# Kernel optimization log

Hardware: AMD Instinct MI355X
Metric: run time of the kernel (lower is better)

Reference implementation:

```python
import jax, jax.numpy as jnp
import numpy as np

EPS = 1e-5

def _bn_relu(y, s, b, m, v):
    # eval-mode BatchNorm1d over channel dim (axis=1) followed by ReLU
    inv = s / jnp.sqrt(v + EPS)
    return jax.nn.relu((y - m[None, :, None]) * inv[None, :, None] + b[None, :, None])

def setup_inputs() -> dict:
    key = jax.random.key(0)
    ks = jax.random.split(key, 24)
    B, C, N, CL = 4, 256, 4096, 32  # CL = C // latent
    x = jax.random.normal(ks[0], (B, C, N), dtype=jnp.float32)
    def w(k, o, i):
        return jax.random.normal(k, (o, i), dtype=jnp.float32) * (1.0 / np.sqrt(i))
    def bn(k0, k1, d):
        s = 1.0 + 0.1 * jax.random.normal(k0, (d,), dtype=jnp.float32)
        b = 0.1 * jax.random.normal(k1, (d,), dtype=jnp.float32)
        m = 0.1 * jax.random.normal(jax.random.fold_in(k0, 7), (d,), dtype=jnp.float32)
        v = 0.5 + jax.random.uniform(jax.random.fold_in(k1, 7), (d,), dtype=jnp.float32)
        return s, b, m, v
    w1 = w(ks[1], CL, C); w2 = w(ks[2], CL, C); w3 = w(ks[3], CL, C)
    w_out = w(ks[4], C, CL)
    bn1_s, bn1_b, bn1_m, bn1_v = bn(ks[5], ks[6], CL)
    bn2_s, bn2_b, bn2_m, bn2_v = bn(ks[7], ks[8], CL)
    bn3_s, bn3_b, bn3_m, bn3_v = bn(ks[9], ks[10], CL)
    bn4_s, bn4_b, bn4_m, bn4_v = bn(ks[11], ks[12], C)
    gamma = jnp.float32(0.5)  # torch inits to 0 (identity output); use 0.5 for a nontrivial baseline
    return dict(x=x, w1=w1, w2=w2, w3=w3, w_out=w_out,
                bn1_s=bn1_s, bn1_b=bn1_b, bn1_m=bn1_m, bn1_v=bn1_v,
                bn2_s=bn2_s, bn2_b=bn2_b, bn2_m=bn2_m, bn2_v=bn2_v,
                bn3_s=bn3_s, bn3_b=bn3_b, bn3_m=bn3_m, bn3_v=bn3_v,
                bn4_s=bn4_s, bn4_b=bn4_b, bn4_m=bn4_m, bn4_v=bn4_v,
                gamma=gamma)

def reference(x, w1, w2, w3, w_out,
              bn1_s, bn1_b, bn1_m, bn1_v,
              bn2_s, bn2_b, bn2_m, bn2_v,
              bn3_s, bn3_b, bn3_m, bn3_v,
              bn4_s, bn4_b, bn4_m, bn4_v,
              gamma):
    # conv1x1 == channel matmul: [o,c] x [b,c,n] -> [b,o,n]
    out1 = _bn_relu(jnp.einsum('oc,bcn->bon', w1, x), bn1_s, bn1_b, bn1_m, bn1_v)  # [b,CL,n]
    out2 = _bn_relu(jnp.einsum('oc,bcn->bon', w2, x), bn2_s, bn2_b, bn2_m, bn2_v)  # [b,CL,n]
    out3 = _bn_relu(jnp.einsum('oc,bcn->bon', w3, x), bn3_s, bn3_b, bn3_m, bn3_v)  # [b,CL,n]
    # attention[b,i,j] = softmax_j( out1[b,:,i] . out2[b,:,j] )
    scores = jnp.einsum('bci,bcj->bij', out1, out2)          # [b,n,n]
    attn = jax.nn.softmax(scores, axis=-1)
    # attention output: bmm(out3, attn^T) -> [b,CL,n]
    agg = jnp.einsum('bck,bmk->bcm', out3, attn)
    out = _bn_relu(jnp.einsum('oc,bcn->bon', w_out, agg), bn4_s, bn4_b, bn4_m, bn4_v)  # [b,C,n]
    return gamma * out + x
```

## Files before the change

### kernel.cpp

```cpp
#include <hip/hip_runtime.h>
#include <hip/hip_bf16.h>
#include <math.h>

#define BATCH 4
#define CDIM 256
#define NDIM 4096
#define CLD 32
#define EPSBN 1e-5f
#define SPLITS 8
#define KEYS_PER_WAVE (NDIM / SPLITS)
#define LOG2E 1.4426950408889634f
#define NT (NDIM / 32)

typedef unsigned short u16;
typedef unsigned int u32;
typedef __attribute__((ext_vector_type(8))) short bf16x8;
typedef __attribute__((ext_vector_type(16))) float f32x16;
typedef __attribute__((ext_vector_type(4))) u32 u32x4;
typedef __attribute__((ext_vector_type(2))) u32 u32x2;

__device__ inline u16 f2bf(float x) {
    return __builtin_bit_cast(u16, __float2bfloat16(x));
}
__device__ inline u32 pack_bf16x2(float a, float b) {
    return (u32)f2bf(a) | ((u32)f2bf(b) << 16);
}
__device__ inline bf16x8 pack8(float4 a, float4 b) {
    u32x4 u;
    u.x = pack_bf16x2(a.x, a.y); u.y = pack_bf16x2(a.z, a.w);
    u.z = pack_bf16x2(b.x, b.y); u.w = pack_bf16x2(b.z, b.w);
    return __builtin_bit_cast(bf16x8, u);
}

__global__ __launch_bounds__(256) void proj_qkv(
    const float* __restrict__ x,
    const float* __restrict__ w1, const float* __restrict__ w2, const float* __restrict__ w3,
    const float* __restrict__ b1s, const float* __restrict__ b1b, const float* __restrict__ b1m, const float* __restrict__ b1v,
    const float* __restrict__ b2s, const float* __restrict__ b2b, const float* __restrict__ b2m, const float* __restrict__ b2v,
    const float* __restrict__ b3s, const float* __restrict__ b3b, const float* __restrict__ b3m, const float* __restrict__ b3v,
    u16* __restrict__ qo, u16* __restrict__ ko, u16* __restrict__ vo)
{
    __shared__ float2 sbn[32];

    const int tid  = threadIdx.x;
    const int lane = tid & 63;
    const int col  = lane & 31;
    const int hi   = lane >> 5;
    const int wv   = tid >> 6;
    const int mat  = blockIdx.y;
    const int b    = blockIdx.z;
    const int tl   = blockIdx.x * 4 + wv;
    const int n0   = tl * 32;

    if (tid < 32) {
        const float* ps = (mat == 0) ? b1s : (mat == 1) ? b2s : b3s;
        const float* pb = (mat == 0) ? b1b : (mat == 1) ? b2b : b3b;
        const float* pm = (mat == 0) ? b1m : (mat == 1) ? b2m : b3m;
        const float* pv = (mat == 0) ? b1v : (mat == 1) ? b2v : b3v;
        float inv  = ps[tid] / sqrtf(pv[tid] + EPSBN);
        float bias = pb[tid] - pm[tid] * inv;
        if (mat == 0) { inv *= LOG2E; bias *= LOG2E; }
        sbn[tid] = make_float2(inv, bias);
    }
    __syncthreads();

    const float* wb = ((mat == 0) ? w1 : (mat == 1) ? w2 : w3) + (size_t)col * CDIM + 8 * hi;
    bf16x8 wf[16];
#pragma unroll
    for (int f = 0; f < 16; ++f) {
        float4 a = *reinterpret_cast<const float4*>(wb + 16 * f);
        float4 c = *reinterpret_cast<const float4*>(wb + 16 * f + 4);
        wf[f] = pack8(a, c);
    }

    const float* xb = x + (size_t)b * CDIM * NDIM + n0 + col;

    f32x16 acc = {0.f,0.f,0.f,0.f, 0.f,0.f,0.f,0.f, 0.f,0.f,0.f,0.f, 0.f,0.f,0.f,0.f};
#pragma unroll
    for (int f = 0; f < 16; ++f) {
        float xv[8];
#pragma unroll
        for (int i = 0; i < 8; ++i)
            xv[i] = xb[(size_t)(16 * f + 8 * hi + i) * NDIM];
        u32x4 u;
        u.x = pack_bf16x2(xv[0], xv[1]); u.y = pack_bf16x2(xv[2], xv[3]);
        u.z = pack_bf16x2(xv[4], xv[5]); u.w = pack_bf16x2(xv[6], xv[7]);
        acc = __builtin_amdgcn_mfma_f32_32x32x16_bf16(wf[f], __builtin_bit_cast(bf16x8, u), acc, 0, 0, 0);
    }

    if (mat < 2) {
        u16* dst = ((mat == 0) ? qo : ko) + ((size_t)b * NDIM + n0 + col) * CLD;
#pragma unroll
        for (int g2 = 0; g2 < 4; ++g2) {
            float y[4];
#pragma unroll
            for (int j = 0; j < 4; ++j) {
                int o = 8 * g2 + 4 * hi + j;
                float2 ib = sbn[o];
                y[j] = fmaxf(fmaf(acc[4 * g2 + j], ib.x, ib.y), 0.f);
            }
            u32x2 s;
            s.x = pack_bf16x2(y[0], y[1]); s.y = pack_bf16x2(y[2], y[3]);
            *reinterpret_cast<u32x2*>(dst + 8 * g2 + 4 * hi) = s;
        }
    } else {
        int p = col;
        int q2 = (p >> 2) & 3;
        if (q2 == 1 || q2 == 2) p ^= 12;
        u16* base = vo + (size_t)(b * NT + tl) * 1024 + p;
#pragma unroll
        for (int r = 0; r < 16; ++r) {
            int d = (r & 3) + 8 * (r >> 2) + 4 * hi;
            float2 ib = sbn[d];
            base[d * 32] = f2bf(fmaxf(fmaf(acc[r], ib.x, ib.y), 0.f));
        }
    }
}

__global__ __launch_bounds__(512, 4) void attn_mfma(
    const u16* __restrict__ q, const u16* __restrict__ k, const u16* __restrict__ v,
    float* __restrict__ agg)
{
    __shared__ float o_lds[SPLITS][32][32];
    __shared__ float l_lds[SPLITS][32];

    const int tid  = threadIdx.x;
    const int lane = tid & 63;
    const int w    = tid >> 6;
    const int b    = blockIdx.y;
    const int q0   = blockIdx.x * 32;
    const int col  = lane & 31;
    const int hi   = lane >> 5;

    const u16* qp = q + ((size_t)b * NDIM + q0 + col) * CLD + 8 * hi;
    bf16x8 qf0 = *reinterpret_cast<const bf16x8*>(qp);
    bf16x8 qf1 = *reinterpret_cast<const bf16x8*>(qp + 16);

    f32x16 o = {0.f,0.f,0.f,0.f, 0.f,0.f,0.f,0.f, 0.f,0.f,0.f,0.f, 0.f,0.f,0.f,0.f};
    float l_lane = 0.f;

    const int kstart = w * KEYS_PER_WAVE;
    const u16* kb = k + (size_t)b * NDIM * CLD;
    const u16* vb = v + (size_t)(b * NT) * 1024 + (size_t)col * 32 + 8 * hi;

    for (int kt = 0; kt < KEYS_PER_WAVE; kt += 64) {
        const int k0 = kstart + kt;
        const u16* kp1 = kb + (size_t)(k0 + col) * CLD + 8 * hi;
        bf16x8 kf10 = *reinterpret_cast<const bf16x8*>(kp1);
        bf16x8 kf11 = *reinterpret_cast<const bf16x8*>(kp1 + 16);
        const u16* kp2 = kp1 + 32 * CLD;
        bf16x8 kf20 = *reinterpret_cast<const bf16x8*>(kp2);
        bf16x8 kf21 = *reinterpret_cast<const bf16x8*>(kp2 + 16);

        const u16* vp = vb + (size_t)(k0 >> 5) * 1024;
        bf16x8 vf10 = *reinterpret_cast<const bf16x8*>(vp);
        bf16x8 vf11 = *reinterpret_cast<const bf16x8*>(vp + 16);
        bf16x8 vf20 = *reinterpret_cast<const bf16x8*>(vp + 1024);
        bf16x8 vf21 = *reinterpret_cast<const bf16x8*>(vp + 1040);

        f32x16 sa = {0.f,0.f,0.f,0.f, 0.f,0.f,0.f,0.f, 0.f,0.f,0.f,0.f, 0.f,0.f,0.f,0.f};
        f32x16 sb = {0.f,0.f,0.f,0.f, 0.f,0.f,0.f,0.f, 0.f,0.f,0.f,0.f, 0.f,0.f,0.f,0.f};
        sa = __builtin_amdgcn_mfma_f32_32x32x16_bf16(kf10, qf0, sa, 0, 0, 0);
        sa = __builtin_amdgcn_mfma_f32_32x32x16_bf16(kf11, qf1, sa, 0, 0, 0);
        sb = __builtin_amdgcn_mfma_f32_32x32x16_bf16(kf20, qf0, sb, 0, 0, 0);
        sb = __builtin_amdgcn_mfma_f32_32x32x16_bf16(kf21, qf1, sb, 0, 0, 0);

        float psum = 0.f;
#pragma unroll
        for (int r = 0; r < 16; ++r) { sa[r] = exp2f(sa[r]); psum += sa[r]; }
#pragma unroll
        for (int r = 0; r < 16; ++r) { sb[r] = exp2f(sb[r]); psum += sb[r]; }
        l_lane += psum;

        u32x4 p10, p11, p20, p21;
        p10.x = pack_bf16x2(sa[0],  sa[1]);  p10.y = pack_bf16x2(sa[2],  sa[3]);
        p10.z = pack_bf16x2(sa[4],  sa[5]);  p10.w = pack_bf16x2(sa[6],  sa[7]);
        p11.x = pack_bf16x2(sa[8],  sa[9]);  p11.y = pack_bf16x2(sa[10], sa[11]);
        p11.z = pack_bf16x2(sa[12], sa[13]); p11.w = pack_bf16x2(sa[14], sa[15]);
        p20.x = pack_bf16x2(sb[0],  sb[1]);  p20.y = pack_bf16x2(sb[2],  sb[3]);
        p20.z = pack_bf16x2(sb[4],  sb[5]);  p20.w = pack_bf16x2(sb[6],  sb[7]);
        p21.x = pack_bf16x2(sb[8],  sb[9]);  p21.y = pack_bf16x2(sb[10], sb[11]);
        p21.z = pack_bf16x2(sb[12], sb[13]); p21.w = pack_bf16x2(sb[14], sb[15]);

        o = __builtin_amdgcn_mfma_f32_32x32x16_bf16(vf10, __builtin_bit_cast(bf16x8, p10), o, 0, 0, 0);
        o = __builtin_amdgcn_mfma_f32_32x32x16_bf16(vf11, __builtin_bit_cast(bf16x8, p11), o, 0, 0, 0);
        o = __builtin_amdgcn_mfma_f32_32x32x16_bf16(vf20, __builtin_bit_cast(bf16x8, p20), o, 0, 0, 0);
        o = __builtin_amdgcn_mfma_f32_32x32x16_bf16(vf21, __builtin_bit_cast(bf16x8, p21), o, 0, 0, 0);
    }

#pragma unroll
    for (int r = 0; r < 16; ++r) {
        int d = (r & 3) + 8 * (r >> 2) + 4 * hi;
        o_lds[w][d][col] = o[r];
    }
    float l_tot = l_lane + __shfl_xor(l_lane, 32);
    if (hi == 0) l_lds[w][col] = l_tot;
    __syncthreads();

    {
        const int qq = tid & 31;
        const int d0 = tid >> 5;
        float den = 0.f;
#pragma unroll
        for (int s = 0; s < SPLITS; ++s) den += l_lds[s][qq];
        float inv = 1.f / den;
#pragma unroll
        for (int dd = 0; dd < 2; ++dd) {
            int d = d0 + 16 * dd;
            float a2 = 0.f;
#pragma unroll
            for (int s = 0; s < SPLITS; ++s) a2 += o_lds[s][d][qq];
            agg[((size_t)b * CLD + d) * NDIM + q0 + qq] = a2 * inv;
        }
    }
}

__global__ __launch_bounds__(256) void out_proj(
    const float* __restrict__ agg, const float* __restrict__ wo,
    const float* __restrict__ b4s, const float* __restrict__ b4b,
    const float* __restrict__ b4m, const float* __restrict__ b4v,
    const float* __restrict__ x, const float* __restrict__ gamma,
    float* __restrict__ out)
{
    const int tid   = threadIdx.x;
    const int lane  = tid & 63;
    const int b     = blockIdx.y;
    const int w     = __builtin_amdgcn_readfirstlane(tid >> 6);
    const int obase = blockIdx.z * 32 + w * 8;
    const int n     = blockIdx.x * 256 + lane * 4;

    float4 acc[8];
#pragma unroll
    for (int o = 0; o < 8; ++o) acc[o] = make_float4(0.f, 0.f, 0.f, 0.f);

    const float* wbase = wo + (size_t)obase * CLD;

#pragma unroll 2
    for (int c = 0; c < CLD; c += 4) {
        float4 wq[8];
#pragma unroll
        for (int o = 0; o < 8; ++o)
            wq[o] = *reinterpret_cast<const float4*>(wbase + o * CLD + c);
        float4 av[4];
#pragma unroll
        for (int cc = 0; cc < 4; ++cc)
            av[cc] = *reinterpret_cast<const float4*>(agg + ((size_t)b * CLD + c + cc) * NDIM + n);
#pragma unroll
        for (int cc = 0; cc < 4; ++cc) {
#pragma unroll
            for (int o = 0; o < 8; ++o) {
                float wv = (cc == 0) ? wq[o].x : (cc == 1) ? wq[o].y : (cc == 2) ? wq[o].z : wq[o].w;
                acc[o].x = fmaf(wv, av[cc].x, acc[o].x);
                acc[o].y = fmaf(wv, av[cc].y, acc[o].y);
                acc[o].z = fmaf(wv, av[cc].z, acc[o].z);
                acc[o].w = fmaf(wv, av[cc].w, acc[o].w);
            }
        }
    }

    const float gm = gamma[0];
#pragma unroll
    for (int o = 0; o < 8; ++o) {
        int oo = obase + o;
        float inv = b4s[oo] / sqrtf(b4v[oo] + EPSBN);
        float bi  = b4b[oo] - b4m[oo] * inv;
        const size_t idx = ((size_t)b * CDIM + oo) * NDIM + n;
        float4 xv = *reinterpret_cast<const float4*>(x + idx);
        float4 r;
        r.x = fmaf(gm, fmaxf(fmaf(acc[o].x, inv, bi), 0.f), xv.x);
        r.y = fmaf(gm, fmaxf(fmaf(acc[o].y, inv, bi), 0.f), xv.y);
        r.z = fmaf(gm, fmaxf(fmaf(acc[o].z, inv, bi), 0.f), xv.z);
        r.w = fmaf(gm, fmaxf(fmaf(acc[o].w, inv, bi), 0.f), xv.w);
        *reinterpret_cast<float4*>(out + idx) = r;
    }
}

extern "C" void kernel_launch(void* const* d_in, const int* in_sizes, int n_in,
                              void* d_out, int out_size, void* d_ws, size_t ws_size,
                              hipStream_t stream) {
    const float* x   = (const float*)d_in[0];
    const float* w1  = (const float*)d_in[1];
    const float* w2  = (const float*)d_in[2];
    const float* w3  = (const float*)d_in[3];
    const float* wo  = (const float*)d_in[4];
    const float* b1s = (const float*)d_in[5];
    const float* b1b = (const float*)d_in[6];
    const float* b1m = (const float*)d_in[7];
    const float* b1v = (const float*)d_in[8];
    const float* b2s = (const float*)d_in[9];
    const float* b2b = (const float*)d_in[10];
    const float* b2m = (const float*)d_in[11];
    const float* b2v = (const float*)d_in[12];
    const float* b3s = (const float*)d_in[13];
    const float* b3b = (const float*)d_in[14];
    const float* b3m = (const float*)d_in[15];
    const float* b3v = (const float*)d_in[16];
    const float* b4s = (const float*)d_in[17];
    const float* b4b = (const float*)d_in[18];
    const float* b4m = (const float*)d_in[19];
    const float* b4v = (const float*)d_in[20];
    const float* gm  = (const float*)d_in[21];
    float* out = (float*)d_out;

    char* W = (char*)d_ws;
    u16* qbf = (u16*)W;
    u16* kbf = (u16*)(W + (1u << 20));
    u16* vbf = (u16*)(W + (2u << 20));
    float* agg = (float*)(W + (3u << 20));

    dim3 gp(32, 3, BATCH);
    proj_qkv<<<gp, 256, 0, stream>>>(x, w1, w2, w3,
                                     b1s, b1b, b1m, b1v,
                                     b2s, b2b, b2m, b2v,
                                     b3s, b3b, b3m, b3v,
                                     qbf, kbf, vbf);

    dim3 ga(NDIM / 32, BATCH);
    attn_mfma<<<ga, 512, 0, stream>>>(qbf, kbf, vbf, agg);

    dim3 go(NDIM / 256, BATCH, 8);
    out_proj<<<go, 256, 0, stream>>>(agg, wo, b4s, b4b, b4m, b4v, x, gm, out);
}
```

Before: 51.02 us.

## Fuse output projection, BN and residual into the attention kernel epilogue

Merges the separate out_proj kernel into the attention kernel. After the split-K reduction, normalized attention outputs are packed to bf16 in LDS, and each wave runs two MFMAs to project 32 latent channels to 32 of the 256 output channels. BN4, ReLU and gamma are applied and staged through LDS, then added to x with coalesced float4 stores. This removes the fp32 agg round trip through global memory and one kernel launch, but the output projection now runs in bf16 instead of fp32 and adds LDS use and extra barriers to the attention kernel.

```diff
diff --git a/kernel.cpp b/kernel.cpp
--- a/kernel.cpp
+++ b/kernel.cpp
@@ -117,12 +117,18 @@
     }
 }
 
-__global__ __launch_bounds__(512, 4) void attn_mfma(
+__global__ __launch_bounds__(512, 4) void attn_fused(
     const u16* __restrict__ q, const u16* __restrict__ k, const u16* __restrict__ v,
-    float* __restrict__ agg)
+    const float* __restrict__ wo,
+    const float* __restrict__ b4s, const float* __restrict__ b4b,
+    const float* __restrict__ b4m, const float* __restrict__ b4v,
+    const float* __restrict__ x, const float* __restrict__ gamma,
+    float* __restrict__ out)
 {
     __shared__ float o_lds[SPLITS][32][32];
     __shared__ float l_lds[SPLITS][32];
+    __shared__ u16  p_lds[32][40];
+    __shared__ float2 sbn4[CDIM];
 
     const int tid  = threadIdx.x;
     const int lane = tid & 63;
@@ -131,6 +137,11 @@
     const int q0   = blockIdx.x * 32;
     const int col  = lane & 31;
     const int hi   = lane >> 5;
+
+    if (tid < CDIM) {
+        float inv = b4s[tid] / sqrtf(b4v[tid] + EPSBN);
+        sbn4[tid] = make_float2(inv, b4b[tid] - b4m[tid] * inv);
+    }
 
     const u16* qp = q + ((size_t)b * NDIM + q0 + col) * CLD + 8 * hi;
     bf16x8 qf0 = *reinterpret_cast<const bf16x8*>(qp);
@@ -199,79 +210,56 @@
 
     {
         const int qq = tid & 31;
-        const int d0 = tid >> 5;
+        const int dp = tid >> 5;
         float den = 0.f;
 #pragma unroll
         for (int s = 0; s < SPLITS; ++s) den += l_lds[s][qq];
         float inv = 1.f / den;
-#pragma unroll
-        for (int dd = 0; dd < 2; ++dd) {
-            int d = d0 + 16 * dd;
-            float a2 = 0.f;
-#pragma unroll
-            for (int s = 0; s < SPLITS; ++s) a2 += o_lds[s][d][qq];
-            agg[((size_t)b * CLD + d) * NDIM + q0 + qq] = a2 * inv;
+        float a0 = 0.f, a1 = 0.f;
+#pragma unroll
+        for (int s = 0; s < SPLITS; ++s) {
+            a0 += o_lds[s][2 * dp][qq];
+            a1 += o_lds[s][2 * dp + 1][qq];
         }
-    }
-}
-
-__global__ __launch_bounds__(256) void out_proj(
-    const float* __restrict__ agg, const float* __restrict__ wo,
-    const float* __restrict__ b4s, const float* __restrict__ b4b,
-    const float* __restrict__ b4m, const float* __restrict__ b4v,
-    const float* __restrict__ x, const float* __restrict__ gamma,
-    float* __restrict__ out)
-{
-    const int tid   = threadIdx.x;
-    const int lane  = tid & 63;
-    const int b     = blockIdx.y;
-    const int w     = __builtin_amdgcn_readfirstlane(tid >> 6);
-    const int obase = blockIdx.z * 32 + w * 8;
-    const int n     = blockIdx.x * 256 + lane * 4;
-
-    float4 acc[8];
-#pragma unroll
-    for (int o = 0; o < 8; ++o) acc[o] = make_float4(0.f, 0.f, 0.f, 0.f);
-
-    const float* wbase = wo + (size_t)obase * CLD;
-
-#pragma unroll 2
-    for (int c = 0; c < CLD; c += 4) {
-        float4 wq[8];
-#pragma unroll
-        for (int o = 0; o < 8; ++o)
-            wq[o] = *reinterpret_cast<const float4*>(wbase + o * CLD + c);
-        float4 av[4];
-#pragma unroll
-        for (int cc = 0; cc < 4; ++cc)
-            av[cc] = *reinterpret_cast<const float4*>(agg + ((size_t)b * CLD + c + cc) * NDIM + n);
-#pragma unroll
-        for (int cc = 0; cc < 4; ++cc) {
-#pragma unroll
-            for (int o = 0; o < 8; ++o) {
-                float wv = (cc == 0) ? wq[o].x : (cc == 1) ? wq[o].y : (cc == 2) ? wq[o].z : wq[o].w;
-                acc[o].x = fmaf(wv, av[cc].x, acc[o].x);
-                acc[o].y = fmaf(wv, av[cc].y, acc[o].y);
-                acc[o].z = fmaf(wv, av[cc].z, acc[o].z);
-                acc[o].w = fmaf(wv, av[cc].w, acc[o].w);
-            }
+        *reinterpret_cast<u32*>(&p_lds[qq][2 * dp]) = pack_bf16x2(a0 * inv, a1 * inv);
+    }
+    __syncthreads();
+
+    const int o0 = w * 32;
+    const float* wp = wo + (size_t)(o0 + col) * CLD + 8 * hi;
+    bf16x8 wf0 = pack8(*reinterpret_cast<const float4*>(wp),
+                       *reinterpret_cast<const float4*>(wp + 4));
+    bf16x8 wf1 = pack8(*reinterpret_cast<const float4*>(wp + 16),
+                       *reinterpret_cast<const float4*>(wp + 20));
+    bf16x8 pf0 = *reinterpret_cast<const bf16x8*>(&p_lds[col][8 * hi]);
+    bf16x8 pf1 = *reinterpret_cast<const bf16x8*>(&p_lds[col][16 + 8 * hi]);
+
+    f32x16 acc = {0.f,0.f,0.f,0.f, 0.f,0.f,0.f,0.f, 0.f,0.f,0.f,0.f, 0.f,0.f,0.f,0.f};
+    acc = __builtin_amdgcn_mfma_f32_32x32x16_bf16(wf0, pf0, acc, 0, 0, 0);
+    acc = __builtin_amdgcn_mfma_f32_32x32x16_bf16(wf1, pf1, acc, 0, 0, 0);
+
+    const float gm = gamma[0];
+#pragma unroll
+    for (int r = 0; r < 16; ++r) {
+        int orow = (r & 3) + 8 * (r >> 2) + 4 * hi;
+        float2 ib = sbn4[o0 + orow];
+        o_lds[w][orow][col] = gm * fmaxf(fmaf(acc[r], ib.x, ib.y), 0.f);
+    }
+    __syncthreads();
+
+    {
+        const int c4 = (lane & 7) * 4;
+#pragma unroll
+        for (int pass = 0; pass < 4; ++pass) {
+            int row = pass * 8 + (lane >> 3);
+            size_t idx = ((size_t)b * CDIM + o0 + row) * NDIM + q0 + c4;
+            float4 yv = *reinterpret_cast<const float4*>(&o_lds[w][row][c4]);
+            float4 xv = *reinterpret_cast<const float4*>(x + idx);
+            float4 rr;
+            rr.x = yv.x + xv.x; rr.y = yv.y + xv.y;
+            rr.z = yv.z + xv.z; rr.w = yv.w + xv.w;
+            *reinterpret_cast<float4*>(out + idx) = rr;
         }
-    }
-
-    const float gm = gamma[0];
-#pragma unroll
-    for (int o = 0; o < 8; ++o) {
-        int oo = obase + o;
-        float inv = b4s[oo] / sqrtf(b4v[oo] + EPSBN);
-        float bi  = b4b[oo] - b4m[oo] * inv;
-        const size_t idx = ((size_t)b * CDIM + oo) * NDIM + n;
-        float4 xv = *reinterpret_cast<const float4*>(x + idx);
-        float4 r;
-        r.x = fmaf(gm, fmaxf(fmaf(acc[o].x, inv, bi), 0.f), xv.x);
-        r.y = fmaf(gm, fmaxf(fmaf(acc[o].y, inv, bi), 0.f), xv.y);
-        r.z = fmaf(gm, fmaxf(fmaf(acc[o].z, inv, bi), 0.f), xv.z);
-        r.w = fmaf(gm, fmaxf(fmaf(acc[o].w, inv, bi), 0.f), xv.w);
-        *reinterpret_cast<float4*>(out + idx) = r;
     }
 }
 
@@ -306,7 +294,6 @@
     u16* qbf = (u16*)W;
     u16* kbf = (u16*)(W + (1u << 20));
     u16* vbf = (u16*)(W + (2u << 20));
-    float* agg = (float*)(W + (3u << 20));
 
     dim3 gp(32, 3, BATCH);
     proj_qkv<<<gp, 256, 0, stream>>>(x, w1, w2, w3,
@@ -316,8 +303,6 @@
                                      qbf, kbf, vbf);
 
     dim3 ga(NDIM / 32, BATCH);
-    attn_mfma<<<ga, 512, 0, stream>>>(qbf, kbf, vbf, agg);
-
-    dim3 go(NDIM / 256, BATCH, 8);
-    out_proj<<<go, 256, 0, stream>>>(agg, wo, b4s, b4b, b4m, b4v, x, gm, out);
-}
+    attn_fused<<<ga, 512, 0, stream>>>(qbf, kbf, vbf, wo, b4s, b4b, b4m, b4v,
+                                       x, gm, out);
+}
```

Result: faster. 45.50 us (-10.8%).
